# Optimization experiments

Hardware: AMD Instinct MI355X
Metric: run time of the kernel (lower is better)

## Reference

```python
import jax, jax.numpy as jnp
import numpy as np

N, E = 20000, 160000
D_IN, HID, HEADS = 256, 64, 10
NEG_SLOPE = 0.2


def setup_inputs() -> dict:
    key = jax.random.key(0)
    ks = jax.random.split(key, 12)
    s = 0.05
    f = jnp.float32
    return {
        "x": jax.random.normal(ks[0], (N, D_IN), f),
        "edge_index": jax.random.randint(ks[1], (2, E), 0, N, jnp.int32),
        # GATConv 1: in=D_IN, out=HID, heads=10, concat=True
        "W1": (jax.random.normal(ks[2], (D_IN, HEADS * HID), f) * s),
        "a_src1": (jax.random.normal(ks[3], (HEADS, HID), f) * s),
        "a_dst1": (jax.random.normal(ks[4], (HEADS, HID), f) * s),
        "b1": jnp.zeros((HEADS * HID,), f),
        # GATConv 2: in=HEADS*HID, out=HID, heads=1
        "W2": (jax.random.normal(ks[5], (HEADS * HID, HID), f) * s),
        "a_src2": (jax.random.normal(ks[6], (1, HID), f) * s),
        "a_dst2": (jax.random.normal(ks[7], (1, HID), f) * s),
        "b2": jnp.zeros((HID,), f),
        # final Linear(hidden_dim, hidden_dim)
        "Wfc": (jax.random.normal(ks[8], (HID, HID), f) * s),
        "bfc": jnp.zeros((HID,), f),
    }


def gat_conv(x, src, dst, n, W, a_src, a_dst, b, heads, concat):
    """PyG GATConv (eval mode): gather, leaky-relu scores, segment softmax, scatter."""
    c = W.shape[1] // heads
    h = (x @ W).reshape(n, heads, c)                      # [N, H, C]
    score_src = jnp.sum(h * a_src, axis=-1)               # [N, H]
    score_dst = jnp.sum(h * a_dst, axis=-1)               # [N, H]
    e = jax.nn.leaky_relu(score_src[src] + score_dst[dst], NEG_SLOPE)  # [E, H]
    # segment softmax over incoming edges of each dst node
    m = jax.ops.segment_max(e, dst, num_segments=n)
    e = jnp.exp(e - m[dst])
    denom = jax.ops.segment_sum(e, dst, num_segments=n)
    alpha = e / (denom[dst] + 1e-16)                      # [E, H]
    msg = alpha[:, :, None] * h[src]                      # [E, H, C]
    out = jax.ops.segment_sum(msg, dst, num_segments=n)   # [N, H, C]
    out = out.reshape(n, heads * c) if concat else out.mean(axis=1)
    return out + b


def reference(x, edge_index, W1, a_src1, a_dst1, b1, W2, a_src2, a_dst2, b2, Wfc, bfc):
    n = x.shape[0]
    # add self loops (PyG default)
    loops = jnp.arange(n, dtype=edge_index.dtype)
    src = jnp.concatenate([edge_index[0], loops])
    dst = jnp.concatenate([edge_index[1], loops])
    h = jax.nn.relu(gat_conv(x, src, dst, n, W1, a_src1, a_dst1, b1, HEADS, True))
    h = jax.nn.relu(gat_conv(h, src, dst, n, W2, a_src2, a_dst2, b2, 1, True))
    return jax.nn.relu(h @ Wfc + bfc)
```

## Files before the change

kernel.cpp:

```cpp
#include <hip/hip_runtime.h>
#include <cstdint>
#include <cstddef>

constexpr int N_NODES = 20000;
constexpr int E_EDGES = 160000;
constexpr int D_INC   = 256;
constexpr int HEADSC  = 10;
constexpr int EN      = E_EDGES + N_NODES;
constexpr int ELLW    = 96;
constexpr float NEG_SLOPE = 0.2f;

typedef _Float16 half8 __attribute__((ext_vector_type(8)));
typedef _Float16 half4v __attribute__((ext_vector_type(4)));
typedef float f32x4 __attribute__((ext_vector_type(4)));

#define GLOBAL_AS const __attribute__((address_space(1))) void*
#define LDS_AS __attribute__((address_space(3))) void*

__global__ __launch_bounds__(256) void gemm1_k(
    const _Float16* __restrict__ A,
    const _Float16* __restrict__ BT,
    _Float16* __restrict__ C,
    const float* __restrict__ asv, const float* __restrict__ adv,
    float* __restrict__ s_s, float* __restrict__ s_d, int M)
{
    __shared__ alignas(16) _Float16 Ah[64][64];
    __shared__ alignas(16) _Float16 Bh[128][64];
    const int tid = threadIdx.x;
    const int wv  = tid >> 6;
    const int ln  = tid & 63;
    const int row0 = blockIdx.y * 64;
    const int col0 = blockIdx.x * 128;
    const int m = ln & 15;
    const int q = ln >> 4;
    const int ar = ln >> 3;
    const int ac = (ln & 7) * 8;

    f32x4 acc[8] = {};

    for (int k0 = 0; k0 < 256; k0 += 64) {
        const _Float16* gp0 = A + (size_t)(row0 + wv * 16 + ar) * 256 + k0 + ac;
        __builtin_amdgcn_global_load_lds((GLOBAL_AS)gp0,
                                         (LDS_AS)&Ah[wv * 16][0], 16, 0, 0);
        __builtin_amdgcn_global_load_lds((GLOBAL_AS)(gp0 + 8 * 256),
                                         (LDS_AS)&Ah[wv * 16 + 8][0], 16, 0, 0);
        const _Float16* gb = BT + (size_t)(col0 + wv * 32 + ar) * 256 + k0 + ac;
#pragma unroll
        for (int jj = 0; jj < 4; ++jj) {
            __builtin_amdgcn_global_load_lds((GLOBAL_AS)(gb + (size_t)jj * 8 * 256),
                                             (LDS_AS)&Bh[wv * 32 + jj * 8][0],
                                             16, 0, 0);
        }
        __syncthreads();
#pragma unroll
        for (int ks = 0; ks < 2; ++ks) {
            const half8 af = *reinterpret_cast<const half8*>(
                &Ah[wv * 16 + m][ks * 32 + q * 8]);
#pragma unroll
            for (int ct = 0; ct < 8; ++ct) {
                const half8 bf = *reinterpret_cast<const half8*>(
                    &Bh[ct * 16 + m][ks * 32 + q * 8]);
                acc[ct] = __builtin_amdgcn_mfma_f32_16x16x32_f16(af, bf, acc[ct],
                                                                 0, 0, 0);
            }
        }
        __syncthreads();
    }

#pragma unroll
    for (int ct = 0; ct < 8; ++ct) {
#pragma unroll
        for (int r = 0; r < 4; ++r) {
            const int row = row0 + wv * 16 + q * 4 + r;
            if (row < M)
                C[(size_t)row * 640 + col0 + ct * 16 + m] = (_Float16)acc[ct][r];
        }
    }

    const int h0 = blockIdx.x * 2;
    float pa[2][4] = {}, pd[2][4] = {};
#pragma unroll
    for (int ct = 0; ct < 8; ++ct) {
        const int hh = ct >> 2;
        const int ch = (ct & 3) * 16 + m;
        const float a_ = asv[(h0 + hh) * 64 + ch];
        const float d_ = adv[(h0 + hh) * 64 + ch];
#pragma unroll
        for (int r = 0; r < 4; ++r) {
            pa[hh][r] += acc[ct][r] * a_;
            pd[hh][r] += acc[ct][r] * d_;
        }
    }
#pragma unroll
    for (int o = 1; o < 16; o <<= 1) {
#pragma unroll
        for (int hh = 0; hh < 2; ++hh)
#pragma unroll
            for (int r = 0; r < 4; ++r) {
                pa[hh][r] += __shfl_xor(pa[hh][r], o, 64);
                pd[hh][r] += __shfl_xor(pd[hh][r], o, 64);
            }
    }
    if (m == 0) {
#pragma unroll
        for (int hh = 0; hh < 2; ++hh)
#pragma unroll
            for (int r = 0; r < 4; ++r) {
                const int row = row0 + wv * 16 + q * 4 + r;
                if (row < M) {
                    s_s[row * HEADSC + h0 + hh] = pa[hh][r];
                    s_d[row * HEADSC + h0 + hh] = pd[hh][r];
                }
            }
    }
}

__global__ __launch_bounds__(128) void gemm_mfma32(
    const _Float16* __restrict__ A,
    const _Float16* __restrict__ BT,
    float* __restrict__ C, int M, int K,
    const float* __restrict__ asv, const float* __restrict__ adv,
    float* __restrict__ s_s, float* __restrict__ s_d)
{
    __shared__ alignas(16) _Float16 Ah[32][32];
    __shared__ alignas(16) _Float16 Bh[64][32];
    const int tid = threadIdx.x;
    const int wv  = tid >> 6;
    const int ln  = tid & 63;
    const int row0 = blockIdx.y * 32;

    f32x4 acc[4] = {};
    const int lr = tid >> 2;
    const int lc = (tid & 3) * 8;
    const int m = ln & 15;
    const int q = ln >> 4;

    for (int k0 = 0; k0 < K; k0 += 32) {
        int4 av = make_int4(0, 0, 0, 0);
        if (row0 + lr < M)
            av = *reinterpret_cast<const int4*>(A + (size_t)(row0 + lr) * K + k0 + lc);
        *reinterpret_cast<int4*>(&Ah[lr][lc]) = av;
        *reinterpret_cast<int4*>(&Bh[lr][lc]) =
            *reinterpret_cast<const int4*>(BT + (size_t)lr * K + k0 + lc);
        *reinterpret_cast<int4*>(&Bh[lr + 32][lc]) =
            *reinterpret_cast<const int4*>(BT + (size_t)(lr + 32) * K + k0 + lc);
        __syncthreads();

        const half8 af = *reinterpret_cast<const half8*>(&Ah[wv * 16 + m][q * 8]);
#pragma unroll
        for (int ct = 0; ct < 4; ++ct) {
            const half8 bf = *reinterpret_cast<const half8*>(&Bh[ct * 16 + m][q * 8]);
            acc[ct] = __builtin_amdgcn_mfma_f32_16x16x32_f16(af, bf, acc[ct], 0, 0, 0);
        }
        __syncthreads();
    }

#pragma unroll
    for (int ct = 0; ct < 4; ++ct) {
#pragma unroll
        for (int r = 0; r < 4; ++r) {
            const int row = row0 + wv * 16 + q * 4 + r;
            if (row < M)
                C[(size_t)row * 64 + ct * 16 + m] = acc[ct][r];
        }
    }

    float pa[4] = {}, pd[4] = {};
#pragma unroll
    for (int ct = 0; ct < 4; ++ct) {
        const float a_ = asv[ct * 16 + m];
        const float d_ = adv[ct * 16 + m];
#pragma unroll
        for (int r = 0; r < 4; ++r) {
            pa[r] += acc[ct][r] * a_;
            pd[r] += acc[ct][r] * d_;
        }
    }
#pragma unroll
    for (int o = 1; o < 16; o <<= 1) {
#pragma unroll
        for (int r = 0; r < 4; ++r) {
            pa[r] += __shfl_xor(pa[r], o, 64);
            pd[r] += __shfl_xor(pd[r], o, 64);
        }
    }
    if (m == 0) {
#pragma unroll
        for (int r = 0; r < 4; ++r) {
            const int row = row0 + wv * 16 + q * 4 + r;
            if (row < M) { s_s[row] = pa[r]; s_d[row] = pd[r]; }
        }
    }
}

constexpr int XQ   = N_NODES * D_INC / 4;
constexpr int W1E  = D_INC * 640;
constexpr int W2E  = 640 * 64;
constexpr int WFCE = 64 * 64;
constexpr int SETUP_TOT = EN + XQ + W1E + W2E + WFCE;

__global__ void setup_k(const int* __restrict__ src, const int* __restrict__ dst,
                        int* __restrict__ deg, int* __restrict__ ell,
                        const float* __restrict__ x, const float* __restrict__ W1,
                        const float* __restrict__ W2, const float* __restrict__ Wfc,
                        _Float16* __restrict__ x16, _Float16* __restrict__ W1T,
                        _Float16* __restrict__ W2T, _Float16* __restrict__ WfcT)
{
    const int i = blockIdx.x * 256 + threadIdx.x;
    if (i < EN) {
        const int base = deg[N_NODES];
        int d, s;
        if (i < E_EDGES) { d = dst[i]; s = src[i]; }
        else             { d = i - E_EDGES; s = d; }
        const int r = atomicAdd(&deg[d], 1) - base;
        if ((unsigned)r < (unsigned)ELLW) ell[(size_t)d * ELLW + r] = s;
    } else if (i < EN + XQ) {
        const int j = i - EN;
        const float4 v = reinterpret_cast<const float4*>(x)[j];
        half4v o = {(_Float16)v.x, (_Float16)v.y, (_Float16)v.z, (_Float16)v.w};
        reinterpret_cast<half4v*>(x16)[j] = o;
    } else if (i < EN + XQ + W1E) {
        const int j = i - EN - XQ;
        const int k = j / 640, n = j - k * 640;
        W1T[(size_t)n * D_INC + k] = (_Float16)W1[j];
    } else if (i < EN + XQ + W1E + W2E) {
        const int j = i - EN - XQ - W1E;
        const int k = j / 64, n = j - k * 64;
        W2T[(size_t)n * 640 + k] = (_Float16)W2[j];
    } else if (i < SETUP_TOT) {
        const int j = i - EN - XQ - W1E - W2E;
        const int k = j >> 6, n = j & 63;
        WfcT[(size_t)n * 64 + k] = (_Float16)Wfc[j];
    }
}

__global__ __launch_bounds__(320) void agg_f16_oct(
    const _Float16* __restrict__ h, const float* __restrict__ s_s,
    const float* __restrict__ s_d, const int* __restrict__ deg,
    const int* __restrict__ ell, const float* __restrict__ bias,
    _Float16* __restrict__ outp)
{
    const int t   = blockIdx.x * 320 + threadIdx.x;
    const int n   = t / 80;
    const int oct = t - n * 80;
    if (n >= N_NODES) return;
    const int hh  = oct >> 3;
    const _Float16* __restrict__ hb = h + oct * 8;
    const int* __restrict__ row = ell + (size_t)n * ELLW;
    const float sd = s_d[n * HEADSC + hh];
    const int dbase = deg[N_NODES];
    const int dc = min(deg[n] - dbase, ELLW);

    float acc[8] = {};
    float den = 0.f;
    int i = 0;
    for (; i + 3 < dc; i += 4) {
        const int s0 = row[i], s1 = row[i + 1], s2 = row[i + 2], s3 = row[i + 3];
        const float g0 = s_s[s0 * HEADSC + hh], g1 = s_s[s1 * HEADSC + hh];
        const float g2 = s_s[s2 * HEADSC + hh], g3 = s_s[s3 * HEADSC + hh];
        const half8 v0 = *reinterpret_cast<const half8*>(hb + (size_t)s0 * 640);
        const half8 v1 = *reinterpret_cast<const half8*>(hb + (size_t)s1 * 640);
        const half8 v2 = *reinterpret_cast<const half8*>(hb + (size_t)s2 * 640);
        const half8 v3 = *reinterpret_cast<const half8*>(hb + (size_t)s3 * 640);
        float e0 = g0 + sd, e1 = g1 + sd, e2 = g2 + sd, e3 = g3 + sd;
        e0 = (e0 > 0.f) ? e0 : NEG_SLOPE * e0;
        e1 = (e1 > 0.f) ? e1 : NEG_SLOPE * e1;
        e2 = (e2 > 0.f) ? e2 : NEG_SLOPE * e2;
        e3 = (e3 > 0.f) ? e3 : NEG_SLOPE * e3;
        const float w0 = __expf(e0), w1 = __expf(e1);
        const float w2 = __expf(e2), w3 = __expf(e3);
        den += (w0 + w1) + (w2 + w3);
#pragma unroll
        for (int j = 0; j < 8; ++j)
            acc[j] += (w0 * (float)v0[j] + w1 * (float)v1[j])
                    + (w2 * (float)v2[j] + w3 * (float)v3[j]);
    }
    for (; i < dc; ++i) {
        const int s0 = row[i];
        const float g0 = s_s[s0 * HEADSC + hh];
        const half8 v0 = *reinterpret_cast<const half8*>(hb + (size_t)s0 * 640);
        float e0 = g0 + sd;
        e0 = (e0 > 0.f) ? e0 : NEG_SLOPE * e0;
        const float w0 = __expf(e0);
        den += w0;
#pragma unroll
        for (int j = 0; j < 8; ++j) acc[j] += w0 * (float)v0[j];
    }
    const float inv = 1.f / (den + 1e-16f);
    const float* bb = bias + oct * 8;
    half8 o;
#pragma unroll
    for (int j = 0; j < 8; ++j)
        o[j] = (_Float16)fmaxf(acc[j] * inv + bb[j], 0.f);
    *reinterpret_cast<half8*>(outp + (size_t)n * 640 + oct * 8) = o;
}

__global__ __launch_bounds__(256) void agg2fc_k(
    const float* __restrict__ h,
    const float* __restrict__ s_s, const float* __restrict__ s_d,
    const int* __restrict__ deg, const int* __restrict__ ell,
    const float* __restrict__ b2,
    const _Float16* __restrict__ WfcT,
    const float* __restrict__ bfc,
    float* __restrict__ out)
{
    __shared__ alignas(16) _Float16 Os[32][72];
    const int tid = threadIdx.x;
    const int n0  = blockIdx.x * 32;
    const int nl  = tid >> 3;
    const int oct = tid & 7;
    const int n   = n0 + nl;

    {
        const float* __restrict__ hb = h + oct * 8;
        const int* __restrict__ row = ell + (size_t)n * ELLW;
        const float sd = s_d[n];
        const int dbase = deg[N_NODES];
        const int dc = min(deg[n] - dbase, ELLW);

        float acc[8] = {};
        float den = 0.f;
        int i = 0;
        for (; i + 1 < dc; i += 2) {
            const int s0 = row[i], s1 = row[i + 1];
            const float g0 = s_s[s0], g1 = s_s[s1];
            const float4 a0 = *reinterpret_cast<const float4*>(hb + (size_t)s0 * 64);
            const float4 a1 = *reinterpret_cast<const float4*>(hb + (size_t)s0 * 64 + 4);
            const float4 b0 = *reinterpret_cast<const float4*>(hb + (size_t)s1 * 64);
            const float4 b1 = *reinterpret_cast<const float4*>(hb + (size_t)s1 * 64 + 4);
            float e0 = g0 + sd, e1 = g1 + sd;
            e0 = (e0 > 0.f) ? e0 : NEG_SLOPE * e0;
            e1 = (e1 > 0.f) ? e1 : NEG_SLOPE * e1;
            const float w0 = __expf(e0), w1 = __expf(e1);
            den += w0 + w1;
            acc[0] += w0 * a0.x + w1 * b0.x; acc[1] += w0 * a0.y + w1 * b0.y;
            acc[2] += w0 * a0.z + w1 * b0.z; acc[3] += w0 * a0.w + w1 * b0.w;
            acc[4] += w0 * a1.x + w1 * b1.x; acc[5] += w0 * a1.y + w1 * b1.y;
            acc[6] += w0 * a1.z + w1 * b1.z; acc[7] += w0 * a1.w + w1 * b1.w;
        }
        if (i < dc) {
            const int s0 = row[i];
            const float g0 = s_s[s0];
            const float4 a0 = *reinterpret_cast<const float4*>(hb + (size_t)s0 * 64);
            const float4 a1 = *reinterpret_cast<const float4*>(hb + (size_t)s0 * 64 + 4);
            float e0 = g0 + sd;
            e0 = (e0 > 0.f) ? e0 : NEG_SLOPE * e0;
            const float w0 = __expf(e0);
            den += w0;
            acc[0] += w0 * a0.x; acc[1] += w0 * a0.y;
            acc[2] += w0 * a0.z; acc[3] += w0 * a0.w;
            acc[4] += w0 * a1.x; acc[5] += w0 * a1.y;
            acc[6] += w0 * a1.z; acc[7] += w0 * a1.w;
        }
        const float inv = 1.f / (den + 1e-16f);
        const float* bb = b2 + oct * 8;
        half8 o;
#pragma unroll
        for (int j = 0; j < 8; ++j)
            o[j] = (_Float16)fmaxf(acc[j] * inv + bb[j], 0.f);
        *reinterpret_cast<half8*>(&Os[nl][oct * 8]) = o;
    }
    __syncthreads();

    const int wv = tid >> 6;
    const int ln = tid & 63;
    if (wv < 2) {
        const int m = ln & 15;
        const int q = ln >> 4;
        f32x4 acc[4] = {};
#pragma unroll
        for (int ks = 0; ks < 2; ++ks) {
            const half8 af = *reinterpret_cast<const half8*>(
                &Os[wv * 16 + m][ks * 32 + q * 8]);
#pragma unroll
            for (int ct = 0; ct < 4; ++ct) {
                const half8 bf = *reinterpret_cast<const half8*>(
                    WfcT + (size_t)(ct * 16 + m) * 64 + ks * 32 + q * 8);
                acc[ct] = __builtin_amdgcn_mfma_f32_16x16x32_f16(af, bf, acc[ct],
                                                                 0, 0, 0);
            }
        }
#pragma unroll
        for (int ct = 0; ct < 4; ++ct) {
#pragma unroll
            for (int r = 0; r < 4; ++r) {
                const int row = n0 + wv * 16 + q * 4 + r;
                const int col = ct * 16 + m;
                out[(size_t)row * 64 + col] = fmaxf(acc[ct][r] + bfc[col], 0.f);
            }
        }
    }
}

extern "C" void kernel_launch(void* const* d_in, const int* in_sizes, int n_in,
                              void* d_out, int out_size, void* d_ws, size_t ws_size,
                              hipStream_t stream)
{
    const float* x      = (const float*)d_in[0];
    const int*   edges  = (const int*)d_in[1];
    const float* W1     = (const float*)d_in[2];
    const float* a_src1 = (const float*)d_in[3];
    const float* a_dst1 = (const float*)d_in[4];
    const float* b1     = (const float*)d_in[5];
    const float* W2     = (const float*)d_in[6];
    const float* a_src2 = (const float*)d_in[7];
    const float* a_dst2 = (const float*)d_in[8];
    const float* b2     = (const float*)d_in[9];
    const float* Wfc    = (const float*)d_in[10];
    const float* bfc    = (const float*)d_in[11];
    float* out = (float*)d_out;

    const int* src = edges;
    const int* dst = edges + E_EDGES;

    char* ws = (char*)d_ws;
    size_t off = 0;
    auto alloc = [&](size_t bytes) -> void* {
        void* p = ws + off;
        off += (bytes + 255) & ~(size_t)255;
        return p;
    };
    _Float16*  h1     = (_Float16*)alloc((size_t)N_NODES * 640 * sizeof(_Float16));
    _Float16*  out1   = (_Float16*)alloc((size_t)N_NODES * 640 * sizeof(_Float16));
    float*     h2     = (float*)alloc((size_t)N_NODES * 64 * sizeof(float));
    _Float16*  x16    = (_Float16*)alloc((size_t)N_NODES * D_INC * sizeof(_Float16));
    _Float16*  W1T    = (_Float16*)alloc((size_t)640 * D_INC * sizeof(_Float16));
    _Float16*  W2T    = (_Float16*)alloc((size_t)64 * 640 * sizeof(_Float16));
    _Float16*  WfcT   = (_Float16*)alloc((size_t)64 * 64 * sizeof(_Float16));
    float*     s_src1 = (float*)alloc((size_t)N_NODES * HEADSC * sizeof(float));
    float*     s_dst1 = (float*)alloc((size_t)N_NODES * HEADSC * sizeof(float));
    float*     s_src2 = (float*)alloc((size_t)N_NODES * sizeof(float));
    float*     s_dst2 = (float*)alloc((size_t)N_NODES * sizeof(float));
    int*       deg    = (int*)alloc((size_t)(N_NODES + 1) * sizeof(int));
    int*       ell    = (int*)alloc((size_t)N_NODES * ELLW * sizeof(int));

    setup_k<<<(SETUP_TOT + 255) / 256, 256, 0, stream>>>(
        src, dst, deg, ell, x, W1, W2, Wfc, x16, W1T, W2T, WfcT);

    dim3 g1(640 / 128, (N_NODES + 63) / 64);
    gemm1_k<<<g1, 256, 0, stream>>>(x16, W1T, h1, a_src1, a_dst1,
                                    s_src1, s_dst1, N_NODES);

    agg_f16_oct<<<(N_NODES * 80) / 320, 320, 0, stream>>>(h1, s_src1, s_dst1, deg,
                                                          ell, b1, out1);

    dim3 g2(1, (N_NODES + 31) / 32);
    gemm_mfma32<<<g2, 128, 0, stream>>>(out1, W2T, h2, N_NODES, 640,
                                        a_src2, a_dst2, s_src2, s_dst2);

    agg2fc_k<<<N_NODES / 32, 256, 0, stream>>>(h2, s_src2, s_dst2, deg, ell,
                                               b2, WfcT, bfc, out);
}
```

Before: 193.9 us.

## Widen GEMM1 tiles, rewrite GEMM2 with LDS-direct loads, store h2 in fp16, unroll gathers

GEMM1 now computes 320 output columns (5 heads) per block instead of 128, so each block reuses its A tile across more columns, at the cost of 20 accumulators and more LDS. GEMM2 is rewritten as a 64-row, 256-thread tile that loads with global_load_lds and writes h2 as fp16, which halves h2 traffic in the second aggregation. The layer-1 aggregation gains an 8-way unrolled gather loop, and the layer-2 aggregation moves to 4-way unrolled fp16 gathers. Register pressure grows in GEMM1, and fp16 h2 lowers precision.

Measured after the change: 199.5 us. +2.9%, slower.

```diff
diff --git a/kernel.cpp b/kernel.cpp
--- a/kernel.cpp
+++ b/kernel.cpp
@@ -25,18 +25,18 @@
     float* __restrict__ s_s, float* __restrict__ s_d, int M)
 {
     __shared__ alignas(16) _Float16 Ah[64][64];
-    __shared__ alignas(16) _Float16 Bh[128][64];
+    __shared__ alignas(16) _Float16 Bh[320][64];
     const int tid = threadIdx.x;
     const int wv  = tid >> 6;
     const int ln  = tid & 63;
     const int row0 = blockIdx.y * 64;
-    const int col0 = blockIdx.x * 128;
+    const int col0 = blockIdx.x * 320;
     const int m = ln & 15;
     const int q = ln >> 4;
     const int ar = ln >> 3;
     const int ac = (ln & 7) * 8;
 
-    f32x4 acc[8] = {};
+    f32x4 acc[20] = {};
 
     for (int k0 = 0; k0 < 256; k0 += 64) {
         const _Float16* gp0 = A + (size_t)(row0 + wv * 16 + ar) * 256 + k0 + ac;
@@ -44,11 +44,11 @@
                                          (LDS_AS)&Ah[wv * 16][0], 16, 0, 0);
         __builtin_amdgcn_global_load_lds((GLOBAL_AS)(gp0 + 8 * 256),
                                          (LDS_AS)&Ah[wv * 16 + 8][0], 16, 0, 0);
-        const _Float16* gb = BT + (size_t)(col0 + wv * 32 + ar) * 256 + k0 + ac;
-#pragma unroll
-        for (int jj = 0; jj < 4; ++jj) {
+        const _Float16* gb = BT + (size_t)(col0 + wv * 80 + ar) * 256 + k0 + ac;
+#pragma unroll
+        for (int jj = 0; jj < 10; ++jj) {
             __builtin_amdgcn_global_load_lds((GLOBAL_AS)(gb + (size_t)jj * 8 * 256),
-                                             (LDS_AS)&Bh[wv * 32 + jj * 8][0],
+                                             (LDS_AS)&Bh[wv * 80 + jj * 8][0],
                                              16, 0, 0);
         }
         __syncthreads();
@@ -57,7 +57,7 @@
             const half8 af = *reinterpret_cast<const half8*>(
                 &Ah[wv * 16 + m][ks * 32 + q * 8]);
 #pragma unroll
-            for (int ct = 0; ct < 8; ++ct) {
+            for (int ct = 0; ct < 20; ++ct) {
                 const half8 bf = *reinterpret_cast<const half8*>(
                     &Bh[ct * 16 + m][ks * 32 + q * 8]);
                 acc[ct] = __builtin_amdgcn_mfma_f32_16x16x32_f16(af, bf, acc[ct],
@@ -68,7 +68,7 @@
     }
 
 #pragma unroll
-    for (int ct = 0; ct < 8; ++ct) {
+    for (int ct = 0; ct < 20; ++ct) {
 #pragma unroll
         for (int r = 0; r < 4; ++r) {
             const int row = row0 + wv * 16 + q * 4 + r;
@@ -77,10 +77,10 @@
         }
     }
 
-    const int h0 = blockIdx.x * 2;
-    float pa[2][4] = {}, pd[2][4] = {};
-#pragma unroll
-    for (int ct = 0; ct < 8; ++ct) {
+    const int h0 = blockIdx.x * 5;
+    float pa[5][4] = {}, pd[5][4] = {};
+#pragma unroll
+    for (int ct = 0; ct < 20; ++ct) {
         const int hh = ct >> 2;
         const int ch = (ct & 3) * 16 + m;
         const float a_ = asv[(h0 + hh) * 64 + ch];
@@ -94,7 +94,7 @@
 #pragma unroll
     for (int o = 1; o < 16; o <<= 1) {
 #pragma unroll
-        for (int hh = 0; hh < 2; ++hh)
+        for (int hh = 0; hh < 5; ++hh)
 #pragma unroll
             for (int r = 0; r < 4; ++r) {
                 pa[hh][r] += __shfl_xor(pa[hh][r], o, 64);
@@ -103,7 +103,7 @@
     }
     if (m == 0) {
 #pragma unroll
-        for (int hh = 0; hh < 2; ++hh)
+        for (int hh = 0; hh < 5; ++hh)
 #pragma unroll
             for (int r = 0; r < 4; ++r) {
                 const int row = row0 + wv * 16 + q * 4 + r;
@@ -115,42 +115,49 @@
     }
 }
 
-__global__ __launch_bounds__(128) void gemm_mfma32(
+__global__ __launch_bounds__(256) void gemm2_k(
     const _Float16* __restrict__ A,
     const _Float16* __restrict__ BT,
-    float* __restrict__ C, int M, int K,
+    _Float16* __restrict__ C,
     const float* __restrict__ asv, const float* __restrict__ adv,
-    float* __restrict__ s_s, float* __restrict__ s_d)
-{
-    __shared__ alignas(16) _Float16 Ah[32][32];
-    __shared__ alignas(16) _Float16 Bh[64][32];
+    float* __restrict__ s_s, float* __restrict__ s_d, int M)
+{
+    __shared__ alignas(16) _Float16 Ah[64][64];
+    __shared__ alignas(16) _Float16 Bh[64][64];
     const int tid = threadIdx.x;
     const int wv  = tid >> 6;
     const int ln  = tid & 63;
-    const int row0 = blockIdx.y * 32;
-
-    f32x4 acc[4] = {};
-    const int lr = tid >> 2;
-    const int lc = (tid & 3) * 8;
+    const int row0 = blockIdx.x * 64;
     const int m = ln & 15;
     const int q = ln >> 4;
-
-    for (int k0 = 0; k0 < K; k0 += 32) {
-        int4 av = make_int4(0, 0, 0, 0);
-        if (row0 + lr < M)
-            av = *reinterpret_cast<const int4*>(A + (size_t)(row0 + lr) * K + k0 + lc);
-        *reinterpret_cast<int4*>(&Ah[lr][lc]) = av;
-        *reinterpret_cast<int4*>(&Bh[lr][lc]) =
-            *reinterpret_cast<const int4*>(BT + (size_t)lr * K + k0 + lc);
-        *reinterpret_cast<int4*>(&Bh[lr + 32][lc]) =
-            *reinterpret_cast<const int4*>(BT + (size_t)(lr + 32) * K + k0 + lc);
+    const int ar = ln >> 3;
+    const int ac = (ln & 7) * 8;
+
+    f32x4 acc[4] = {};
+
+    for (int k0 = 0; k0 < 640; k0 += 64) {
+        const _Float16* gp0 = A + (size_t)(row0 + wv * 16 + ar) * 640 + k0 + ac;
+        __builtin_amdgcn_global_load_lds((GLOBAL_AS)gp0,
+                                         (LDS_AS)&Ah[wv * 16][0], 16, 0, 0);
+        __builtin_amdgcn_global_load_lds((GLOBAL_AS)(gp0 + 8 * 640),
+                                         (LDS_AS)&Ah[wv * 16 + 8][0], 16, 0, 0);
+        const _Float16* gb = BT + (size_t)(wv * 16 + ar) * 640 + k0 + ac;
+        __builtin_amdgcn_global_load_lds((GLOBAL_AS)gb,
+                                         (LDS_AS)&Bh[wv * 16][0], 16, 0, 0);
+        __builtin_amdgcn_global_load_lds((GLOBAL_AS)(gb + 8 * 640),
+                                         (LDS_AS)&Bh[wv * 16 + 8][0], 16, 0, 0);
         __syncthreads();
-
-        const half8 af = *reinterpret_cast<const half8*>(&Ah[wv * 16 + m][q * 8]);
-#pragma unroll
-        for (int ct = 0; ct < 4; ++ct) {
-            const half8 bf = *reinterpret_cast<const half8*>(&Bh[ct * 16 + m][q * 8]);
-            acc[ct] = __builtin_amdgcn_mfma_f32_16x16x32_f16(af, bf, acc[ct], 0, 0, 0);
+#pragma unroll
+        for (int ks = 0; ks < 2; ++ks) {
+            const half8 af = *reinterpret_cast<const half8*>(
+                &Ah[wv * 16 + m][ks * 32 + q * 8]);
+#pragma unroll
+            for (int ct = 0; ct < 4; ++ct) {
+                const half8 bf = *reinterpret_cast<const half8*>(
+                    &Bh[ct * 16 + m][ks * 32 + q * 8]);
+                acc[ct] = __builtin_amdgcn_mfma_f32_16x16x32_f16(af, bf, acc[ct],
+                                                                 0, 0, 0);
+            }
         }
         __syncthreads();
     }
@@ -161,7 +168,7 @@
         for (int r = 0; r < 4; ++r) {
             const int row = row0 + wv * 16 + q * 4 + r;
             if (row < M)
-                C[(size_t)row * 64 + ct * 16 + m] = acc[ct][r];
+                C[(size_t)row * 64 + ct * 16 + m] = (_Float16)acc[ct][r];
         }
     }
 
@@ -254,26 +261,47 @@
     float acc[8] = {};
     float den = 0.f;
     int i = 0;
+    for (; i + 7 < dc; i += 8) {
+        int   sv[8];
+        float gv[8];
+        half8 hv[8];
+#pragma unroll
+        for (int u = 0; u < 8; ++u) sv[u] = row[i + u];
+#pragma unroll
+        for (int u = 0; u < 8; ++u) gv[u] = s_s[sv[u] * HEADSC + hh];
+#pragma unroll
+        for (int u = 0; u < 8; ++u)
+            hv[u] = *reinterpret_cast<const half8*>(hb + (size_t)sv[u] * 640);
+#pragma unroll
+        for (int u = 0; u < 8; ++u) {
+            float e = gv[u] + sd;
+            e = (e > 0.f) ? e : NEG_SLOPE * e;
+            const float w = __expf(e);
+            den += w;
+#pragma unroll
+            for (int j = 0; j < 8; ++j) acc[j] += w * (float)hv[u][j];
+        }
+    }
     for (; i + 3 < dc; i += 4) {
-        const int s0 = row[i], s1 = row[i + 1], s2 = row[i + 2], s3 = row[i + 3];
-        const float g0 = s_s[s0 * HEADSC + hh], g1 = s_s[s1 * HEADSC + hh];
-        const float g2 = s_s[s2 * HEADSC + hh], g3 = s_s[s3 * HEADSC + hh];
-        const half8 v0 = *reinterpret_cast<const half8*>(hb + (size_t)s0 * 640);
-        const half8 v1 = *reinterpret_cast<const half8*>(hb + (size_t)s1 * 640);
-        const half8 v2 = *reinterpret_cast<const half8*>(hb + (size_t)s2 * 640);
-        const half8 v3 = *reinterpret_cast<const half8*>(hb + (size_t)s3 * 640);
-        float e0 = g0 + sd, e1 = g1 + sd, e2 = g2 + sd, e3 = g3 + sd;
-        e0 = (e0 > 0.f) ? e0 : NEG_SLOPE * e0;
-        e1 = (e1 > 0.f) ? e1 : NEG_SLOPE * e1;
-        e2 = (e2 > 0.f) ? e2 : NEG_SLOPE * e2;
-        e3 = (e3 > 0.f) ? e3 : NEG_SLOPE * e3;
-        const float w0 = __expf(e0), w1 = __expf(e1);
-        const float w2 = __expf(e2), w3 = __expf(e3);
-        den += (w0 + w1) + (w2 + w3);
-#pragma unroll
-        for (int j = 0; j < 8; ++j)
-            acc[j] += (w0 * (float)v0[j] + w1 * (float)v1[j])
-                    + (w2 * (float)v2[j] + w3 * (float)v3[j]);
+        int   sv[4];
+        float gv[4];
+        half8 hv[4];
+#pragma unroll
+        for (int u = 0; u < 4; ++u) sv[u] = row[i + u];
+#pragma unroll
+        for (int u = 0; u < 4; ++u) gv[u] = s_s[sv[u] * HEADSC + hh];
+#pragma unroll
+        for (int u = 0; u < 4; ++u)
+            hv[u] = *reinterpret_cast<const half8*>(hb + (size_t)sv[u] * 640);
+#pragma unroll
+        for (int u = 0; u < 4; ++u) {
+            float e = gv[u] + sd;
+            e = (e > 0.f) ? e : NEG_SLOPE * e;
+            const float w = __expf(e);
+            den += w;
+#pragma unroll
+            for (int j = 0; j < 8; ++j) acc[j] += w * (float)hv[u][j];
+        }
     }
     for (; i < dc; ++i) {
         const int s0 = row[i];
@@ -296,7 +324,7 @@
 }
 
 __global__ __launch_bounds__(256) void agg2fc_k(
-    const float* __restrict__ h,
+    const _Float16* __restrict__ h,
     const float* __restrict__ s_s, const float* __restrict__ s_d,
     const int* __restrict__ deg, const int* __restrict__ ell,
     const float* __restrict__ b2,
@@ -312,7 +340,7 @@
     const int n   = n0 + nl;
 
     {
-        const float* __restrict__ hb = h + oct * 8;
+        const _Float16* __restrict__ hb = h + oct * 8;
         const int* __restrict__ row = ell + (size_t)n * ELLW;
         const float sd = s_d[n];
         const int dbase = deg[N_NODES];
@@ -321,36 +349,37 @@
         float acc[8] = {};
         float den = 0.f;
         int i = 0;
-        for (; i + 1 < dc; i += 2) {
-            const int s0 = row[i], s1 = row[i + 1];
-            const float g0 = s_s[s0], g1 = s_s[s1];
-            const float4 a0 = *reinterpret_cast<const float4*>(hb + (size_t)s0 * 64);
-            const float4 a1 = *reinterpret_cast<const float4*>(hb + (size_t)s0 * 64 + 4);
-            const float4 b0 = *reinterpret_cast<const float4*>(hb + (size_t)s1 * 64);
-            const float4 b1 = *reinterpret_cast<const float4*>(hb + (size_t)s1 * 64 + 4);
-            float e0 = g0 + sd, e1 = g1 + sd;
-            e0 = (e0 > 0.f) ? e0 : NEG_SLOPE * e0;
-            e1 = (e1 > 0.f) ? e1 : NEG_SLOPE * e1;
-            const float w0 = __expf(e0), w1 = __expf(e1);
-            den += w0 + w1;
-            acc[0] += w0 * a0.x + w1 * b0.x; acc[1] += w0 * a0.y + w1 * b0.y;
-            acc[2] += w0 * a0.z + w1 * b0.z; acc[3] += w0 * a0.w + w1 * b0.w;
-            acc[4] += w0 * a1.x + w1 * b1.x; acc[5] += w0 * a1.y + w1 * b1.y;
-            acc[6] += w0 * a1.z + w1 * b1.z; acc[7] += w0 * a1.w + w1 * b1.w;
-        }
-        if (i < dc) {
+        for (; i + 3 < dc; i += 4) {
+            int   sv[4];
+            float gv[4];
+            half8 hv[4];
+#pragma unroll
+            for (int u = 0; u < 4; ++u) sv[u] = row[i + u];
+#pragma unroll
+            for (int u = 0; u < 4; ++u) gv[u] = s_s[sv[u]];
+#pragma unroll
+            for (int u = 0; u < 4; ++u)
+                hv[u] = *reinterpret_cast<const half8*>(hb + (size_t)sv[u] * 64);
+#pragma unroll
+            for (int u = 0; u < 4; ++u) {
+                float e = gv[u] + sd;
+                e = (e > 0.f) ? e : NEG_SLOPE * e;
+                const float w = __expf(e);
+                den += w;
+#pragma unroll
+                for (int j = 0; j < 8; ++j) acc[j] += w * (float)hv[u][j];
+            }
+        }
+        for (; i < dc; ++i) {
             const int s0 = row[i];
             const float g0 = s_s[s0];
-            const float4 a0 = *reinterpret_cast<const float4*>(hb + (size_t)s0 * 64);
-            const float4 a1 = *reinterpret_cast<const float4*>(hb + (size_t)s0 * 64 + 4);
+            const half8 v0 = *reinterpret_cast<const half8*>(hb + (size_t)s0 * 64);
             float e0 = g0 + sd;
             e0 = (e0 > 0.f) ? e0 : NEG_SLOPE * e0;
             const float w0 = __expf(e0);
             den += w0;
-            acc[0] += w0 * a0.x; acc[1] += w0 * a0.y;
-            acc[2] += w0 * a0.z; acc[3] += w0 * a0.w;
-            acc[4] += w0 * a1.x; acc[5] += w0 * a1.y;
-            acc[6] += w0 * a1.z; acc[7] += w0 * a1.w;
+#pragma unroll
+            for (int j = 0; j < 8; ++j) acc[j] += w0 * (float)v0[j];
         }
         const float inv = 1.f / (den + 1e-16f);
         const float* bb = b2 + oct * 8;
@@ -422,7 +451,7 @@
     };
     _Float16*  h1     = (_Float16*)alloc((size_t)N_NODES * 640 * sizeof(_Float16));
     _Float16*  out1   = (_Float16*)alloc((size_t)N_NODES * 640 * sizeof(_Float16));
-    float*     h2     = (float*)alloc((size_t)N_NODES * 64 * sizeof(float));
+    _Float16*  h2     = (_Float16*)alloc((size_t)N_NODES * 64 * sizeof(_Float16));
     _Float16*  x16    = (_Float16*)alloc((size_t)N_NODES * D_INC * sizeof(_Float16));
     _Float16*  W1T    = (_Float16*)alloc((size_t)640 * D_INC * sizeof(_Float16));
     _Float16*  W2T    = (_Float16*)alloc((size_t)64 * 640 * sizeof(_Float16));
@@ -437,16 +466,16 @@
     setup_k<<<(SETUP_TOT + 255) / 256, 256, 0, stream>>>(
         src, dst, deg, ell, x, W1, W2, Wfc, x16, W1T, W2T, WfcT);
 
-    dim3 g1(640 / 128, (N_NODES + 63) / 64);
+    dim3 g1(2, (N_NODES + 63) / 64);
     gemm1_k<<<g1, 256, 0, stream>>>(x16, W1T, h1, a_src1, a_dst1,
                                     s_src1, s_dst1, N_NODES);
 
     agg_f16_oct<<<(N_NODES * 80) / 320, 320, 0, stream>>>(h1, s_src1, s_dst1, deg,
                                                           ell, b1, out1);
 
-    dim3 g2(1, (N_NODES + 31) / 32);
-    gemm_mfma32<<<g2, 128, 0, stream>>>(out1, W2T, h2, N_NODES, 640,
-                                        a_src2, a_dst2, s_src2, s_dst2);
+    gemm2_k<<<(N_NODES + 63) / 64, 256, 0, stream>>>(out1, W2T, h2,
+                                                     a_src2, a_dst2,
+                                                     s_src2, s_dst2, N_NODES);
 
     agg2fc_k<<<N_NODES / 32, 256, 0, stream>>>(h2, s_src2, s_dst2, deg, ell,
                                                b2, WfcT, bfc, out);
```
